# Performance work log

Measured on AMD Instinct MI355X. Metric: run time of the kernel, lower is better.

The kernel has to match this reference:

```python
import jax, jax.numpy as jnp
import numpy as np

B, S, D_MODEL = 2, 2048, 2048
N_HEADS, N_KV_HEADS, D_HEAD = 32, 8, 64
INIT_STD = 0.02


def setup_inputs() -> dict:
    key = jax.random.key(0)
    k1, k2, k3, k4, k5 = jax.random.split(key, 5)
    return {
        "residual": jax.random.normal(k1, (B, S, D_MODEL), dtype=jnp.float32),
        "W_Q": jax.random.normal(k2, (N_HEADS, D_HEAD, D_MODEL), dtype=jnp.float32) * INIT_STD,
        "W_K": jax.random.normal(k3, (N_KV_HEADS, D_HEAD, D_MODEL), dtype=jnp.float32) * INIT_STD,
        "W_V": jax.random.normal(k4, (N_KV_HEADS, D_HEAD, D_MODEL), dtype=jnp.float32) * INIT_STD,
        "W_O": jax.random.normal(k5, (N_HEADS, D_HEAD, D_MODEL), dtype=jnp.float32) * INIT_STD,
    }


def reference(residual, W_Q, W_K, W_V, W_O):
    # QKV projections: residual [b,p,d] x W [n,h,d] -> [b,p,n,h]
    q = jnp.einsum('bpd,nhd->bpnh', residual, W_Q)
    k = jnp.einsum('bpd,nhd->bpnh', residual, W_K)
    v = jnp.einsum('bpd,nhd->bpnh', residual, W_V)

    # GQA: repeat_interleave kv heads up to n_heads
    rep = N_HEADS // N_KV_HEADS
    k = jnp.repeat(k, rep, axis=2)  # [b, p, n_heads, h]
    v = jnp.repeat(v, rep, axis=2)

    # scaled dot-product scores: [b, n, q, k]
    scores = jnp.einsum('bqnh,bknh->bnqk', q, k) / jnp.sqrt(jnp.float32(D_HEAD))

    # causal mask (seq_len == total_len, no cache)
    seq_len = residual.shape[1]
    causal = jnp.tril(jnp.ones((seq_len, seq_len), dtype=bool))
    scores = jnp.where(causal[None, None, :, :], scores, jnp.float32(-jnp.inf))

    pattern = jax.nn.softmax(scores, axis=-1)

    # weighted sum of values: [b, q, n, h]
    attn_out = jnp.einsum('bnqk,bknh->bqnh', pattern, v)

    # output projection: [b, q, d_model]
    out = jnp.einsum('bqnh,nhd->bqd', attn_out, W_O)
    return out
```

## Files before the change

kernel.cpp:

```cpp
#include <hip/hip_runtime.h>


typedef __attribute__((ext_vector_type(8))) short short8;
typedef __attribute__((ext_vector_type(4))) short short4v;
typedef __attribute__((ext_vector_type(4))) float f32x4;

__device__ __forceinline__ short f2bs(float f) {
  unsigned u = __float_as_uint(f);
  u = (u + 0x7fffu + ((u >> 16) & 1u)) >> 16;
  return (short)u;
}
__device__ __forceinline__ float bs2f(short s) {
  return __uint_as_float(((unsigned)(unsigned short)s) << 16);
}

__device__ __forceinline__ void async_ld16(const void* g, void* l) {
  __builtin_amdgcn_global_load_lds((__attribute__((address_space(1))) void*)(g),
                                   (__attribute__((address_space(3))) void*)(l),
                                   16, 0, 0);
}

#define BARRIER()                       \
  do {                                  \
    asm volatile("" ::: "memory");      \
    __builtin_amdgcn_s_barrier();       \
    asm volatile("" ::: "memory");      \
  } while (0)
#define LGKM0()                                          \
  do {                                                   \
    asm volatile("s_waitcnt lgkmcnt(0)" ::: "memory");   \
    __builtin_amdgcn_sched_barrier(0);                   \
  } while (0)
#define VMCNT(n) asm volatile("s_waitcnt vmcnt(" #n ")" ::: "memory")
#define MFMA16(a, b, c) \
  (c) = __builtin_amdgcn_mfma_f32_16x16x32_bf16((a), (b), (c), 0, 0, 0)

__device__ __forceinline__ short4v pk4bf16(float p0, float p1, float p2,
                                           float p3) {
  union {
    unsigned u[2];
    short4v s;
  } pk;
  asm("v_cvt_pk_bf16_f32 %0, %1, %2" : "=v"(pk.u[0]) : "v"(p0), "v"(p1));
  asm("v_cvt_pk_bf16_f32 %0, %1, %2" : "=v"(pk.u[1]) : "v"(p2), "v"(p3));
  return pk.s;
}

__device__ __forceinline__ int block_sniff_f32(const short* __restrict__ r,
                                               int* bad) {
  if (threadIdx.x == 0) *bad = 0;
  __syncthreads();
  int my = 0;
  for (int i = threadIdx.x; i < 512; i += blockDim.x) {
    float x = bs2f(r[i]);
    if (!(fabsf(x) < 100.0f)) my = 1;
  }
  if (my) atomicOr(bad, 1);
  __syncthreads();
  return *bad;
}

__global__ __launch_bounds__(256) void prep_kernel(
    const void* __restrict__ s0, const void* __restrict__ s1,
    const void* __restrict__ s2, const void* __restrict__ s3,
    short* __restrict__ d0, short* __restrict__ d1, short* __restrict__ d2,
    short* __restrict__ d3, const void* __restrict__ wo,
    short* __restrict__ wot) {
  __shared__ short tile[64][65];
  __shared__ int badsh;
  const int isf = block_sniff_f32((const short*)s0, &badsh);
  const int bid = blockIdx.x;
  if (bid < 7168) {
    long off = (long)bid * 256 + threadIdx.x;
    const void* src;
    short* dst;
    if (off < 1048576) {
      src = s0; dst = d0;
    } else if ((off -= 1048576) < 524288) {
      src = s1; dst = d1;
    } else if ((off -= 524288) < 131072) {
      src = s2; dst = d2;
    } else {
      off -= 131072; src = s3; dst = d3;
    }
    const long e = off * 8;
    short8 v;
    if (isf) {
      const float* f = (const float*)src + e;
      const f32x4 a = *(const f32x4*)(f);
      const f32x4 b = *(const f32x4*)(f + 4);
#pragma unroll
      for (int j = 0; j < 4; ++j) {
        v[j] = f2bs(a[j]);
        v[4 + j] = f2bs(b[j]);
      }
    } else {
      v = *(const short8*)((const short*)src + e);
    }
    *(short8*)(dst + e) = v;
  } else {
    const int tb = bid - 7168;
    const int bx = tb & 31, by = tb >> 5;
    const int tx = threadIdx.x & 63, ty = threadIdx.x >> 6;
#pragma unroll
    for (int i = 0; i < 16; ++i) {
      const int r = ty + i * 4;
      const size_t idx = (size_t)(by * 64 + r) * 2048 + bx * 64 + tx;
      tile[r][tx] =
          isf ? f2bs(((const float*)wo)[idx]) : ((const short*)wo)[idx];
    }
    __syncthreads();
#pragma unroll
    for (int i = 0; i < 16; ++i) {
      const int r = ty + i * 4;
      wot[(size_t)(bx * 64 + r) * 2048 + by * 64 + tx] = tile[tx][r];
    }
  }
}

__device__ __forceinline__ void gemm256(const short* __restrict__ A, int lda,
                                        const short* __restrict__ B, int ldb,
                                        void* __restrict__ C, int ldc,
                                        int rowBase, int colBase, int K,
                                        short* SM, int outF32, float cscale) {
  const int t = threadIdx.x;
  const int wave = t >> 6;
  const int lane = t & 63;
  const int quad = lane >> 4;
  const int m16 = lane & 15;
  const int wr = (wave >> 2) * 128;
  const int wc = (wave & 3) * 64;

  short* const As0 = SM;
  short* const As1 = SM + 16384;
  short* const Bs0 = SM + 32768;
  short* const Bs1 = SM + 49152;

  const int sr = t >> 3;
  const int sc8 = ((t & 7) ^ (sr & 7)) * 8;
  const short* aS = A + (size_t)(rowBase + sr) * lda + sc8;
  const short* bS = B + (size_t)(colBase + sr) * ldb + sc8;
  const int dOff = wave * 512;

#define STG_A(buf, rg, kt) \
  async_ld16(aS + (size_t)(rg) * lda + (kt) * 64, (buf) + (rg) * 64 + dOff)
#define STG_B(buf, rg, kt) \
  async_ld16(bS + (size_t)(rg) * ldb + (kt) * 64, (buf) + (rg) * 64 + dOff)
#define RD(buf, row0, kh)                          \
  (*(const short8*)((buf) + ((row0) + m16) * 64 +  \
                    ((((kh) * 4 + quad) ^ (m16 & 7)) * 8)))

  const int nT = K >> 6;
  STG_A(As0, 0, 0); STG_A(As0, 64, 0); STG_A(As0, 128, 0); STG_A(As0, 192, 0);
  STG_B(Bs0, 0, 0); STG_B(Bs0, 64, 0); STG_B(Bs0, 128, 0); STG_B(Bs0, 192, 0);
  if (nT > 1) {
    STG_A(As1, 0, 1); STG_A(As1, 64, 1); STG_A(As1, 128, 1); STG_A(As1, 192, 1);
  }

  f32x4 acc[8][4] = {};
  for (int tt = 0; tt < nT; ++tt) {
    short* const Ac = (tt & 1) ? As1 : As0;
    short* const Bc = (tt & 1) ? Bs1 : Bs0;
    short* const Bn = (tt & 1) ? Bs0 : Bs1;

    if (tt + 1 < nT) {
      VMCNT(4);
    } else {
      VMCNT(0);
    }
    BARRIER();

    short8 alo[4][2], blo[2][2];
#pragma unroll
    for (int i = 0; i < 4; ++i) {
      alo[i][0] = RD(Ac, wr + i * 16, 0);
      alo[i][1] = RD(Ac, wr + i * 16, 1);
    }
#pragma unroll
    for (int j = 0; j < 2; ++j) {
      blo[j][0] = RD(Bc, wc + j * 16, 0);
      blo[j][1] = RD(Bc, wc + j * 16, 1);
    }
    if (tt + 1 < nT) { STG_B(Bn, 0, tt + 1); STG_B(Bn, 64, tt + 1); }
    BARRIER();
    LGKM0();
    __builtin_amdgcn_s_setprio(1);
#pragma unroll
    for (int i = 0; i < 4; ++i)
#pragma unroll
      for (int j = 0; j < 2; ++j) {
        MFMA16(alo[i][0], blo[j][0], acc[i][j]);
        MFMA16(alo[i][1], blo[j][1], acc[i][j]);
      }
    __builtin_amdgcn_s_setprio(0);
    BARRIER();

    short8 bhi[2][2];
#pragma unroll
    for (int j = 0; j < 2; ++j) {
      bhi[j][0] = RD(Bc, wc + 32 + j * 16, 0);
      bhi[j][1] = RD(Bc, wc + 32 + j * 16, 1);
    }
    if (tt + 1 < nT) { STG_B(Bn, 128, tt + 1); STG_B(Bn, 192, tt + 1); }
    BARRIER();
    LGKM0();
    __builtin_amdgcn_s_setprio(1);
#pragma unroll
    for (int i = 0; i < 4; ++i)
#pragma unroll
      for (int j = 0; j < 2; ++j) {
        MFMA16(alo[i][0], bhi[j][0], acc[i][2 + j]);
        MFMA16(alo[i][1], bhi[j][1], acc[i][2 + j]);
      }
    __builtin_amdgcn_s_setprio(0);
    BARRIER();

    short8 ahi[4][2];
#pragma unroll
    for (int i = 0; i < 4; ++i) {
      ahi[i][0] = RD(Ac, wr + 64 + i * 16, 0);
      ahi[i][1] = RD(Ac, wr + 64 + i * 16, 1);
    }
    BARRIER();
    if (tt + 2 < nT) { STG_A(Ac, 0, tt + 2); STG_A(Ac, 64, tt + 2); }
    LGKM0();
    __builtin_amdgcn_s_setprio(1);
#pragma unroll
    for (int i = 0; i < 4; ++i)
#pragma unroll
      for (int j = 0; j < 2; ++j) {
        MFMA16(ahi[i][0], blo[j][0], acc[4 + i][j]);
        MFMA16(ahi[i][1], blo[j][1], acc[4 + i][j]);
      }
    __builtin_amdgcn_s_setprio(0);
    BARRIER();

    if (tt + 2 < nT) { STG_A(Ac, 128, tt + 2); STG_A(Ac, 192, tt + 2); }
    __builtin_amdgcn_s_setprio(1);
#pragma unroll
    for (int i = 0; i < 4; ++i)
#pragma unroll
      for (int j = 0; j < 2; ++j) {
        MFMA16(ahi[i][0], bhi[j][0], acc[4 + i][2 + j]);
        MFMA16(ahi[i][1], bhi[j][1], acc[4 + i][2 + j]);
      }
    __builtin_amdgcn_s_setprio(0);
  }

  float* const F = (float*)SM + wave * 4096;
#pragma unroll
  for (int h = 0; h < 2; ++h) {
    if (h) LGKM0();
#pragma unroll
    for (int i = 0; i < 4; ++i)
#pragma unroll
      for (int j = 0; j < 4; ++j)
#pragma unroll
        for (int r = 0; r < 4; ++r)
          F[(i * 16 + quad * 4 + r) * 64 + j * 16 + m16] =
              acc[h * 4 + i][j][r] * cscale;
    LGKM0();
#pragma unroll
    for (int p = 0; p < 16; ++p) {
      const int row = p * 4 + quad;
      const f32x4 vv = *(const f32x4*)(F + row * 64 + m16 * 4);
      const size_t gi =
          (size_t)(rowBase + wr + h * 64 + row) * ldc + colBase + wc + m16 * 4;
      if (outF32) {
        *(f32x4*)((float*)C + gi) = vv;
      } else {
        short4v s;
#pragma unroll
        for (int r = 0; r < 4; ++r) s[r] = f2bs(vv[r]);
        *(short4v*)((short*)C + gi) = s;
      }
    }
  }
#undef STG_A
#undef STG_B
#undef RD
}

__device__ __forceinline__ void gemm256x128(const short* __restrict__ A,
                                            int lda,
                                            const short* __restrict__ B,
                                            int ldb, void* __restrict__ C,
                                            int ldc, int rowBase, int colBase,
                                            int K, short* SM, int outF32) {
  const int t = threadIdx.x;
  const int wave = t >> 6;
  const int lane = t & 63;
  const int quad = lane >> 4;
  const int m16 = lane & 15;
  const int wr = (wave >> 1) * 64;
  const int wc = (wave & 1) * 64;

  short* const As0 = SM;
  short* const As1 = SM + 16384;
  short* const Bs0 = SM + 32768;
  short* const Bs1 = SM + 40960;

  const int sr = t >> 3;
  const int sc8 = ((t & 7) ^ (sr & 7)) * 8;
  const short* aS = A + (size_t)(rowBase + sr) * lda + sc8;
  const short* bS = B + (size_t)(colBase + sr) * ldb + sc8;
  const int dOff = wave * 512;

#define STG_A(buf, rg, kt) \
  async_ld16(aS + (size_t)(rg) * lda + (kt) * 64, (buf) + (rg) * 64 + dOff)
#define STG_B(buf, rg, kt) \
  async_ld16(bS + (size_t)(rg) * ldb + (kt) * 64, (buf) + (rg) * 64 + dOff)
#define RD(buf, row0, kh)                          \
  (*(const short8*)((buf) + ((row0) + m16) * 64 +  \
                    ((((kh) * 4 + quad) ^ (m16 & 7)) * 8)))

  const int nT = K >> 6;
  STG_A(As0, 0, 0); STG_A(As0, 64, 0); STG_A(As0, 128, 0); STG_A(As0, 192, 0);
  STG_B(Bs0, 0, 0); STG_B(Bs0, 64, 0);
  if (nT > 1) {
    STG_A(As1, 0, 1); STG_A(As1, 64, 1); STG_A(As1, 128, 1); STG_A(As1, 192, 1);
  }

  f32x4 acc[4][4] = {};
  for (int tt = 0; tt < nT; ++tt) {
    short* const Ac = (tt & 1) ? As1 : As0;
    short* const Bc = (tt & 1) ? Bs1 : Bs0;
    short* const Bn = (tt & 1) ? Bs0 : Bs1;

    if (tt + 1 < nT) {
      VMCNT(4);
    } else {
      VMCNT(0);
    }
    BARRIER();

    short8 a0[4], b0[4];
#pragma unroll
    for (int i = 0; i < 4; ++i) a0[i] = RD(Ac, wr + i * 16, 0);
#pragma unroll
    for (int j = 0; j < 4; ++j) b0[j] = RD(Bc, wc + j * 16, 0);
    if (tt + 1 < nT) { STG_B(Bn, 0, tt + 1); STG_B(Bn, 64, tt + 1); }
    BARRIER();
    LGKM0();
    __builtin_amdgcn_s_setprio(1);
#pragma unroll
    for (int i = 0; i < 4; ++i)
#pragma unroll
      for (int j = 0; j < 4; ++j) MFMA16(a0[i], b0[j], acc[i][j]);
    __builtin_amdgcn_s_setprio(0);
    BARRIER();

    short8 a1[4], b1[4];
#pragma unroll
    for (int i = 0; i < 4; ++i) a1[i] = RD(Ac, wr + i * 16, 1);
#pragma unroll
    for (int j = 0; j < 4; ++j) b1[j] = RD(Bc, wc + j * 16, 1);
    BARRIER();
    LGKM0();
    __builtin_amdgcn_s_setprio(1);
#pragma unroll
    for (int i = 0; i < 4; ++i)
#pragma unroll
      for (int j = 0; j < 4; ++j) MFMA16(a1[i], b1[j], acc[i][j]);
    __builtin_amdgcn_s_setprio(0);
    BARRIER();

    if (tt + 2 < nT) {
      STG_A(Ac, 0, tt + 2); STG_A(Ac, 64, tt + 2);
      STG_A(Ac, 128, tt + 2); STG_A(Ac, 192, tt + 2);
    }
  }

  float* const F = (float*)SM + wave * 4096;
#pragma unroll
  for (int i = 0; i < 4; ++i)
#pragma unroll
    for (int j = 0; j < 4; ++j)
#pragma unroll
      for (int r = 0; r < 4; ++r)
        F[(i * 16 + quad * 4 + r) * 64 + j * 16 + m16] = acc[i][j][r];
  LGKM0();
#pragma unroll
  for (int p = 0; p < 16; ++p) {
    const int row = p * 4 + quad;
    const f32x4 vv = *(const f32x4*)(F + row * 64 + m16 * 4);
    const size_t gi =
        (size_t)(rowBase + wr + row) * ldc + colBase + wc + m16 * 4;
    if (outF32) {
      *(f32x4*)((float*)C + gi) = vv;
    } else {
      short4v s;
#pragma unroll
      for (int r = 0; r < 4; ++r) s[r] = f2bs(vv[r]);
      *(short4v*)((short*)C + gi) = s;
    }
  }
#undef STG_A
#undef STG_B
#undef RD
}

__global__ __launch_bounds__(512, 2) void qkv_gemm_kernel(
    const short* __restrict__ R, const short* __restrict__ WQ,
    const short* __restrict__ WK, const short* __restrict__ WV,
    short* __restrict__ q, short* __restrict__ k, short* __restrict__ v) {
  __shared__ __align__(16) short SM[65536];
  const int lid = blockIdx.x;
  const int nl = (lid & 7) * 24 + (lid >> 3);
  const int ct = nl % 12;
  const int rt = nl / 12;
  const short* Bm;
  short* Cout;
  int colBase, ldc;
  float cs = 1.0f;
  if (ct < 8) {
    Bm = WQ; Cout = q; colBase = ct * 256; ldc = 2048;
    cs = 0.125f * 1.44269504088896340736f;
  } else if (ct < 10) {
    Bm = WK; Cout = k; colBase = (ct - 8) * 256; ldc = 512;
  } else {
    Bm = WV; Cout = v; colBase = (ct - 10) * 256; ldc = 512;
  }
  gemm256(R, 2048, Bm, 2048, Cout, ldc, rt * 256, colBase, 2048, SM, 0, cs);
}

__global__ __launch_bounds__(512, 2) void out_gemm_kernel(
    const short* __restrict__ A, const short* __restrict__ Bt,
    void* __restrict__ C, const short* __restrict__ sniffsrc) {
  __shared__ __align__(16) short SM[65536];
  const int outF32 = block_sniff_f32(sniffsrc, (int*)SM);
  const int lid = blockIdx.x;
  const int nl = (lid & 7) * 32 + (lid >> 3);
  const int ct = nl & 15;
  const int rt = nl >> 4;
  gemm256x128(A, 2048, Bt, 2048, C, 2048, rt * 256, ct * 128, 2048, SM,
              outF32);
}

__global__ __launch_bounds__(256) void vt_kernel(const short* __restrict__ v,
                                                 short* __restrict__ vt) {
  __shared__ short tile[64][65];
  const int hb = blockIdx.x * 64, pb = blockIdx.y * 64, b = blockIdx.z;
  const int tx = threadIdx.x & 63, ty = threadIdx.x >> 6;
#pragma unroll
  for (int i = 0; i < 16; ++i) {
    const int r = ty + i * 4;
    tile[r][tx] = v[((size_t)(b * 2048 + pb + r)) * 512 + hb + tx];
  }
  __syncthreads();
#pragma unroll
  for (int i = 0; i < 16; ++i) {
    const int r = ty + i * 4;
    vt[((size_t)(b * 512 + hb + r)) * 2048 + pb + tx] = tile[tx][r];
  }
}

__global__ __launch_bounds__(256, 3) void attn_kernel(
    const short* __restrict__ qbuf, const short* __restrict__ kbuf,
    const short* __restrict__ vtb, short* __restrict__ obuf) {
  __shared__ __align__(16) short Ks[2][64 * 64];
  __shared__ __align__(16) short Vs[2][64 * 64];
  __shared__ __align__(16) short Pb[4][32 * 64];

  const int b = blockIdx.x >> 3;
  const int kv = blockIdx.x & 7;
  const int qc = 63 - blockIdx.y;
  const int t = threadIdx.x;
  const int wave = t >> 6;
  const int hd = kv * 4 + wave;
  const int lane = t & 63;
  const int quad = lane >> 4;
  const int col = lane & 15;
  const int rb0 = qc * 32;

  short8 qf[2][2];
#pragma unroll
  for (int nt = 0; nt < 2; ++nt) {
    const int qr = rb0 + nt * 16 + col;
    const short* qp = qbuf + ((size_t)(b * 2048 + qr)) * 2048 + hd * 64 + quad * 8;
    qf[nt][0] = *(const short8*)(qp);
    qf[nt][1] = *(const short8*)(qp + 32);
  }

  short8 ones;
#pragma unroll
  for (int i = 0; i < 8; ++i) ones[i] = (short)0x3F80;

  f32x4 oacc[2][4] = {};
  f32x4 sacc[2] = {};

  short* P = &Pb[wave][0];
  const int swz = 4 * (col & 3);

  const int sRow = t >> 3;
  const int sPos = t & 7;
  const int r1 = sRow + 32;
  const short* kRow0 = kbuf + ((size_t)(b * 2048 + sRow)) * 512 + kv * 64 +
                       ((sPos ^ (sRow & 7)) * 8);
  const short* kRow1 = kbuf + ((size_t)(b * 2048 + r1)) * 512 + kv * 64 +
                       ((sPos ^ (r1 & 7)) * 8);
  const short* vRow0 = vtb + ((size_t)(b * 512 + kv * 64 + sRow)) * 2048 +
                       ((sPos ^ (sRow & 7)) * 8);
  const short* vRow1 = vtb + ((size_t)(b * 512 + kv * 64 + r1)) * 2048 +
                       ((sPos ^ (r1 & 7)) * 8);

  const int nkt = (qc >> 1) + 1;

  async_ld16(kRow0, &Ks[0][wave * 512]);
  async_ld16(kRow1, &Ks[0][2048 + wave * 512]);
  async_ld16(vRow0, &Vs[0][wave * 512]);
  async_ld16(vRow1, &Vs[0][2048 + wave * 512]);

  for (int kt = 0; kt < nkt; ++kt) {
    __syncthreads();
    if (kt + 1 < nkt) {
      const int nb = (kt + 1) & 1;
      const size_t ko = (size_t)(kt + 1) * 64 * 512;
      const int vo = (kt + 1) * 64;
      async_ld16(kRow0 + ko, &Ks[nb][wave * 512]);
      async_ld16(kRow1 + ko, &Ks[nb][2048 + wave * 512]);
      async_ld16(vRow0 + vo, &Vs[nb][wave * 512]);
      async_ld16(vRow1 + vo, &Vs[nb][2048 + wave * 512]);
    }
    const int ktb = kt * 64;
    const short* ks = &Ks[kt & 1][0];
    const short* vs = &Vs[kt & 1][0];

    short8 kf[4][2];
#pragma unroll
    for (int mt = 0; mt < 4; ++mt) {
      const int krow = mt * 16 + col;
      kf[mt][0] = *(const short8*)(ks + krow * 64 + ((quad ^ (col & 7)) * 8));
      kf[mt][1] = *(const short8*)(ks + krow * 64 + (((4 + quad) ^ (col & 7)) * 8));
    }

#pragma unroll
    for (int nt = 0; nt < 2; ++nt) {
      const int rb = rb0 + nt * 16;

      f32x4 st[4];
#pragma unroll
      for (int mt = 0; mt < 4; ++mt) {
        f32x4 z = {0.f, 0.f, 0.f, 0.f};
        z = __builtin_amdgcn_mfma_f32_16x16x32_bf16(kf[mt][0], qf[nt][0], z, 0, 0, 0);
        z = __builtin_amdgcn_mfma_f32_16x16x32_bf16(kf[mt][1], qf[nt][1], z, 0, 0, 0);
        st[mt] = z;
      }

      if (ktb + 63 > rb) {
        const int qrow = rb + col;
#pragma unroll
        for (int mt = 0; mt < 4; ++mt)
#pragma unroll
          for (int r = 0; r < 4; ++r)
            if (ktb + mt * 16 + quad * 4 + r > qrow) st[mt][r] = -1.0e30f;
      }

#pragma unroll
      for (int mt = 0; mt < 4; ++mt) {
        const float p0 = exp2f(st[mt][0]);
        const float p1 = exp2f(st[mt][1]);
        const float p2 = exp2f(st[mt][2]);
        const float p3 = exp2f(st[mt][3]);
        *(short4v*)(P + (nt * 16 + col) * 64 + (quad + 4 * (mt ^ (col & 3))) * 4) =
            pk4bf16(p0, p1, p2, p3);
      }
    }

    asm volatile("s_waitcnt lgkmcnt(0)" ::: "memory");

    short8 pf[2][2];
#pragma unroll
    for (int nt = 0; nt < 2; ++nt) {
      const int base = (nt * 16 + col) * 64;
      pf[nt][0] = *(const short8*)(P + base + ((2 * quad) ^ swz) * 4);
      pf[nt][1] = *(const short8*)(P + base + ((8 + 2 * quad) ^ swz) * 4);
    }

#pragma unroll
    for (int nt = 0; nt < 2; ++nt) {
      sacc[nt] = __builtin_amdgcn_mfma_f32_16x16x32_bf16(ones, pf[nt][0],
                                                         sacc[nt], 0, 0, 0);
      sacc[nt] = __builtin_amdgcn_mfma_f32_16x16x32_bf16(ones, pf[nt][1],
                                                         sacc[nt], 0, 0, 0);
    }

#pragma unroll
    for (int ct = 0; ct < 4; ++ct) {
      const int h = ct * 16 + col;
      const short8 va = *(const short8*)(vs + h * 64 + ((quad ^ (col & 7)) * 8));
      const short8 vb = *(const short8*)(vs + h * 64 + (((4 + quad) ^ (col & 7)) * 8));
#pragma unroll
      for (int nt = 0; nt < 2; ++nt) {
        oacc[nt][ct] = __builtin_amdgcn_mfma_f32_16x16x32_bf16(
            va, pf[nt][0], oacc[nt][ct], 0, 0, 0);
        oacc[nt][ct] = __builtin_amdgcn_mfma_f32_16x16x32_bf16(
            vb, pf[nt][1], oacc[nt][ct], 0, 0, 0);
      }
    }
  }

  const float inv0 = 1.0f / sacc[0][0];
  const float inv1 = 1.0f / sacc[1][0];
#pragma unroll
  for (int nt = 0; nt < 2; ++nt) {
    const float inv = nt ? inv1 : inv0;
#pragma unroll
    for (int ct = 0; ct < 4; ++ct) {
      *(short4v*)(P + (nt * 16 + col) * 64 + ct * 16 + quad * 4) =
          pk4bf16(oacc[nt][ct][0] * inv, oacc[nt][ct][1] * inv,
                  oacc[nt][ct][2] * inv, oacc[nt][ct][3] * inv);
    }
  }
  asm volatile("s_waitcnt lgkmcnt(0)" ::: "memory");
#pragma unroll
  for (int p = 0; p < 4; ++p) {
    const int qlocal = (lane >> 3) + 8 * p;
    const short8 row = *(const short8*)(P + qlocal * 64 + (lane & 7) * 8);
    *(short8*)(obuf + ((size_t)(b * 2048 + rb0 + qlocal)) * 2048 + hd * 64 +
               (lane & 7) * 8) = row;
  }
}

extern "C" void kernel_launch(void* const* d_in, const int* in_sizes, int n_in,
                              void* d_out, int out_size, void* d_ws,
                              size_t ws_size, hipStream_t stream) {
  char* ws = (char*)d_ws;
  short* rbuf = (short*)(ws + 256);
  short* wqb = rbuf + 8388608;
  short* wkb = wqb + 4194304;
  short* wvb = wkb + 1048576;
  short* kbuf = wvb + 1048576;
  short* vbuf = kbuf + 2097152;
  short* abuf = vbuf + 2097152;
  short* wot = abuf + 8388608;
  short* vtb = wqb;
  short* qbuf = (short*)d_out;

  hipLaunchKernelGGL(prep_kernel, dim3(8192), dim3(256), 0, stream,
                     d_in[0], d_in[1], d_in[2], d_in[3], rbuf, wqb, wkb, wvb,
                     d_in[4], wot);
  hipLaunchKernelGGL(qkv_gemm_kernel, dim3(192), dim3(512), 0, stream,
                     rbuf, wqb, wkb, wvb, qbuf, kbuf, vbuf);
  hipLaunchKernelGGL(vt_kernel, dim3(8, 32, 2), dim3(256), 0, stream,
                     vbuf, vtb);
  hipLaunchKernelGGL(attn_kernel, dim3(16, 64), dim3(256), 0, stream,
                     qbuf, kbuf, vtb, abuf);
  hipLaunchKernelGGL(out_gemm_kernel, dim3(256), dim3(512), 0, stream,
                     abuf, wot, (void*)d_out, (const short*)d_in[0]);
}
```

Before: 280.8 us.

## Drop per-phase barriers and setprio in GEMM main loops, issue prefetches early

Both GEMM main loops are restructured so that next-tile B loads are issued right after the top barrier, and all LDS fragment reads and MFMAs run without the intermediate barriers and s_setprio toggles. Only one LGKM wait plus barrier remains before the A buffer is overwritten, so per-iteration synchronisation drops from several barriers to two. This removes wave-lockstep stalls and lets the compiler interleave reads with MFMAs. The cost is the loss of the ping-pong scheduling between waves that the priority toggles provided, and less control over how LDS traffic and MFMAs overlap.

```diff
diff --git a/kernel.cpp b/kernel.cpp
--- a/kernel.cpp
+++ b/kernel.cpp
@@ -170,7 +170,12 @@
     }
     BARRIER();
 
-    short8 alo[4][2], blo[2][2];
+    if (tt + 1 < nT) {
+      STG_B(Bn, 0, tt + 1); STG_B(Bn, 64, tt + 1);
+      STG_B(Bn, 128, tt + 1); STG_B(Bn, 192, tt + 1);
+    }
+
+    short8 alo[4][2], blo[2][2], bhi[2][2];
 #pragma unroll
     for (int i = 0; i < 4; ++i) {
       alo[i][0] = RD(Ac, wr + i * 16, 0);
@@ -181,10 +186,6 @@
       blo[j][0] = RD(Bc, wc + j * 16, 0);
       blo[j][1] = RD(Bc, wc + j * 16, 1);
     }
-    if (tt + 1 < nT) { STG_B(Bn, 0, tt + 1); STG_B(Bn, 64, tt + 1); }
-    BARRIER();
-    LGKM0();
-    __builtin_amdgcn_s_setprio(1);
 #pragma unroll
     for (int i = 0; i < 4; ++i)
 #pragma unroll
@@ -192,19 +193,11 @@
         MFMA16(alo[i][0], blo[j][0], acc[i][j]);
         MFMA16(alo[i][1], blo[j][1], acc[i][j]);
       }
-    __builtin_amdgcn_s_setprio(0);
-    BARRIER();
-
-    short8 bhi[2][2];
 #pragma unroll
     for (int j = 0; j < 2; ++j) {
       bhi[j][0] = RD(Bc, wc + 32 + j * 16, 0);
       bhi[j][1] = RD(Bc, wc + 32 + j * 16, 1);
     }
-    if (tt + 1 < nT) { STG_B(Bn, 128, tt + 1); STG_B(Bn, 192, tt + 1); }
-    BARRIER();
-    LGKM0();
-    __builtin_amdgcn_s_setprio(1);
 #pragma unroll
     for (int i = 0; i < 4; ++i)
 #pragma unroll
@@ -212,8 +205,6 @@
         MFMA16(alo[i][0], bhi[j][0], acc[i][2 + j]);
         MFMA16(alo[i][1], bhi[j][1], acc[i][2 + j]);
       }
-    __builtin_amdgcn_s_setprio(0);
-    BARRIER();
 
     short8 ahi[4][2];
 #pragma unroll
@@ -221,10 +212,14 @@
       ahi[i][0] = RD(Ac, wr + 64 + i * 16, 0);
       ahi[i][1] = RD(Ac, wr + 64 + i * 16, 1);
     }
+    LGKM0();
     BARRIER();
-    if (tt + 2 < nT) { STG_A(Ac, 0, tt + 2); STG_A(Ac, 64, tt + 2); }
-    LGKM0();
-    __builtin_amdgcn_s_setprio(1);
+
+    if (tt + 2 < nT) {
+      STG_A(Ac, 0, tt + 2); STG_A(Ac, 64, tt + 2);
+      STG_A(Ac, 128, tt + 2); STG_A(Ac, 192, tt + 2);
+    }
+
 #pragma unroll
     for (int i = 0; i < 4; ++i)
 #pragma unroll
@@ -232,11 +227,6 @@
         MFMA16(ahi[i][0], blo[j][0], acc[4 + i][j]);
         MFMA16(ahi[i][1], blo[j][1], acc[4 + i][j]);
       }
-    __builtin_amdgcn_s_setprio(0);
-    BARRIER();
-
-    if (tt + 2 < nT) { STG_A(Ac, 128, tt + 2); STG_A(Ac, 192, tt + 2); }
-    __builtin_amdgcn_s_setprio(1);
 #pragma unroll
     for (int i = 0; i < 4; ++i)
 #pragma unroll
@@ -244,7 +234,6 @@
         MFMA16(ahi[i][0], bhi[j][0], acc[4 + i][2 + j]);
         MFMA16(ahi[i][1], bhi[j][1], acc[4 + i][2 + j]);
       }
-    __builtin_amdgcn_s_setprio(0);
   }
 
   float* const F = (float*)SM + wave * 4096;
@@ -334,41 +323,35 @@
     }
     BARRIER();
 
+    if (tt + 1 < nT) { STG_B(Bn, 0, tt + 1); STG_B(Bn, 64, tt + 1); }
+
     short8 a0[4], b0[4];
 #pragma unroll
     for (int i = 0; i < 4; ++i) a0[i] = RD(Ac, wr + i * 16, 0);
 #pragma unroll
     for (int j = 0; j < 4; ++j) b0[j] = RD(Bc, wc + j * 16, 0);
-    if (tt + 1 < nT) { STG_B(Bn, 0, tt + 1); STG_B(Bn, 64, tt + 1); }
-    BARRIER();
+#pragma unroll
+    for (int i = 0; i < 4; ++i)
+#pragma unroll
+      for (int j = 0; j < 4; ++j) MFMA16(a0[i], b0[j], acc[i][j]);
+
+    short8 a1[4], b1[4];
+#pragma unroll
+    for (int i = 0; i < 4; ++i) a1[i] = RD(Ac, wr + i * 16, 1);
+#pragma unroll
+    for (int j = 0; j < 4; ++j) b1[j] = RD(Bc, wc + j * 16, 1);
     LGKM0();
-    __builtin_amdgcn_s_setprio(1);
-#pragma unroll
-    for (int i = 0; i < 4; ++i)
-#pragma unroll
-      for (int j = 0; j < 4; ++j) MFMA16(a0[i], b0[j], acc[i][j]);
-    __builtin_amdgcn_s_setprio(0);
-    BARRIER();
-
-    short8 a1[4], b1[4];
-#pragma unroll
-    for (int i = 0; i < 4; ++i) a1[i] = RD(Ac, wr + i * 16, 1);
-#pragma unroll
-    for (int j = 0; j < 4; ++j) b1[j] = RD(Bc, wc + j * 16, 1);
-    BARRIER();
-    LGKM0();
-    __builtin_amdgcn_s_setprio(1);
-#pragma unroll
-    for (int i = 0; i < 4; ++i)
-#pragma unroll
-      for (int j = 0; j < 4; ++j) MFMA16(a1[i], b1[j], acc[i][j]);
-    __builtin_amdgcn_s_setprio(0);
     BARRIER();
 
     if (tt + 2 < nT) {
       STG_A(Ac, 0, tt + 2); STG_A(Ac, 64, tt + 2);
       STG_A(Ac, 128, tt + 2); STG_A(Ac, 192, tt + 2);
     }
+
+#pragma unroll
+    for (int i = 0; i < 4; ++i)
+#pragma unroll
+      for (int j = 0; j < 4; ++j) MFMA16(a1[i], b1[j], acc[i][j]);
   }
 
   float* const F = (float*)SM + wave * 4096;
```

After: 280.6 us. Within noise of the previous version (-0.1%).
